# Optimization experiments

Hardware: AMD Instinct MI355X
Metric: run time of the kernel (lower is better)

Reference implementation:

```python
import jax, jax.numpy as jnp
import numpy as np

N = 2048          # num_nodes
A = 100           # anchor count (hard-coded in _select_anchor_points)


def setup_inputs() -> dict:
    key = jax.random.key(0)
    k1, k2, k3 = jax.random.split(key, 3)
    motifGraph = jax.random.uniform(k1, (N, N), dtype=jnp.float32)
    node_weights = jax.random.uniform(k2, (N,), dtype=jnp.float32)
    weight_matrix = jax.random.uniform(k3, (N, A), dtype=jnp.float32)
    sigma = jnp.array(1.0, dtype=jnp.float32)
    return {"motifGraph": motifGraph, "node_weights": node_weights,
            "weight_matrix": weight_matrix, "sigma": sigma}


def _floyd_warshall(w):
    # w: [n,n] edge-weight matrix (inf = no edge, 0 on diagonal)
    n = w.shape[0]
    def step(d, k):
        # d_ij = min(d_ij, d_ik + d_kj)
        d = jnp.minimum(d, d[:, k][:, None] + d[k, :][None, :])
        return d, None
    d, _ = jax.lax.scan(step, w, jnp.arange(n))
    return d


def reference(motifGraph, node_weights, weight_matrix, sigma):
    n = motifGraph.shape[0]
    # _adjust_motif_graph: row-scale by node weights. The original detaches
    # before the scipy floyd_warshall call, so no grad flows through it.
    adj = jax.lax.stop_gradient(motifGraph * node_weights[:n, None])
    # csr_matrix semantics: zero entries are "no edge"; directed=False takes
    # the min of w_ij and w_ji; diagonal distance is 0.
    w = jnp.where(adj > 0, adj, jnp.inf)
    w = jnp.minimum(w, w.T)
    idx = jnp.arange(n)
    w = w.at[idx, idx].set(0.0)
    dist = _floyd_warshall(w)
    dist = jnp.where(jnp.isinf(dist), 100.0, dist)
    # _select_anchor_points: top-100 node weights (all indices < n here)
    anchors = jnp.argsort(-jax.lax.stop_gradient(node_weights))[:A]
    consensus_vectors = dist[:, anchors]                      # [n, A]
    distance_sums = (consensus_vectors.sum(axis=1) - 100.0).sum() / (n * A)
    weighted = weight_matrix[:n, :] * consensus_vectors       # [n, A]
    # build_consensus_graph: cdist(...)**4 == (squared euclidean dist)**2
    xx = jnp.sum(weighted * weighted, axis=1)                 # [n]
    sq = jnp.maximum(xx[:, None] + xx[None, :] - 2.0 * weighted @ weighted.T, 0.0)
    consensus_graph = jnp.exp(-(sq * sq) / (2.0 * sigma ** 2))
    return consensus_vectors, distance_sums, consensus_graph
```

## Files before the change

### kernel.cpp

```cpp
#include <hip/hip_runtime.h>
#include <stdint.h>

#define NN 2048
#define AA 100
#define NT 32

#define F_DIAG   256
#define F_ROW    512
#define F_COL    1536
#define F_PREROW 2560
#define F_PRECOL 2624

typedef float floatx4 __attribute__((ext_vector_type(4)));

template<bool AL> __device__ __forceinline__ float4 ld4(const float* __restrict__ p) {
  if (AL) return *(const float4*)p;
  return make_float4(p[0], p[1], p[2], p[3]);
}
template<bool AL> __device__ __forceinline__ void st4(float* __restrict__ p, float4 v) {
  if (AL) { *(float4*)p = v; }
  else { p[0] = v.x; p[1] = v.y; p[2] = v.z; p[3] = v.w; }
}

__device__ __forceinline__ void minplus16(const float (*A)[68], const float (*B)[68],
                                          float c[4][4], int i0, int j0) {
#pragma unroll 4
  for (int k4 = 0; k4 < 16; ++k4) {
    const int k = k4 * 4;
    float4 a0 = *(const float4*)&A[i0 + 0][k];
    float4 a1 = *(const float4*)&A[i0 + 1][k];
    float4 a2 = *(const float4*)&A[i0 + 2][k];
    float4 a3 = *(const float4*)&A[i0 + 3][k];
    float4 b0 = *(const float4*)&B[k + 0][j0];
    float4 b1 = *(const float4*)&B[k + 1][j0];
    float4 b2 = *(const float4*)&B[k + 2][j0];
    float4 b3 = *(const float4*)&B[k + 3][j0];
#define MP1(ii, jj, f)                                                           \
    c[ii][jj] = fminf(fminf(fminf(fminf(c[ii][jj], a##ii.x + b0.f),              \
                                  a##ii.y + b1.f),                               \
                            a##ii.z + b2.f),                                     \
                      a##ii.w + b3.f)
#define MP_ROW(ii) MP1(ii, 0, x); MP1(ii, 1, y); MP1(ii, 2, z); MP1(ii, 3, w)
    MP_ROW(0); MP_ROW(1); MP_ROW(2); MP_ROW(3);
#undef MP_ROW
#undef MP1
  }
}

__device__ __forceinline__ void close_seq(float (*S)[68], float c[4][4],
                                          int i0, int j0, int ty, int tx) {
  for (int kb = 0; kb < 16; ++kb) {
#pragma unroll
    for (int h = 0; h < 2; ++h) {
      const int k = kb * 4 + h * 2;
      float4 br  = *(const float4*)&S[k][j0];
      float4 br2 = *(const float4*)&S[k + 1][j0];
      float dkk1 = S[k][k + 1];
      float dk1k = S[k + 1][k];
      float a0 = S[i0 + 0][k],     a1 = S[i0 + 1][k],
            a2 = S[i0 + 2][k],     a3 = S[i0 + 3][k];
      float e0 = S[i0 + 0][k + 1], e1 = S[i0 + 1][k + 1],
            e2 = S[i0 + 2][k + 1], e3 = S[i0 + 3][k + 1];
      float4 brp;
      brp.x = fminf(br2.x, dk1k + br.x);
      brp.y = fminf(br2.y, dk1k + br.y);
      brp.z = fminf(br2.z, dk1k + br.z);
      brp.w = fminf(br2.w, dk1k + br.w);
      e0 = fminf(e0, a0 + dkk1);
      e1 = fminf(e1, a1 + dkk1);
      e2 = fminf(e2, a2 + dkk1);
      e3 = fminf(e3, a3 + dkk1);
#define CS2(ii, aa, ee)                                                     \
      c[ii][0] = fminf(fminf(c[ii][0], aa + br.x), ee + brp.x);             \
      c[ii][1] = fminf(fminf(c[ii][1], aa + br.y), ee + brp.y);             \
      c[ii][2] = fminf(fminf(c[ii][2], aa + br.z), ee + brp.z);             \
      c[ii][3] = fminf(fminf(c[ii][3], aa + br.w), ee + brp.w)
      CS2(0, a0, e0); CS2(1, a1, e1); CS2(2, a2, e2); CS2(3, a3, e3);
#undef CS2
      const int kn = k + 2;
      if (kn < 64) {
        const int ow = kn >> 2;
        const int ri = (h == 0) ? 2 : 0;
        if (ow == ty) {
          *(float4*)&S[kn][j0] =
              make_float4(c[ri][0], c[ri][1], c[ri][2], c[ri][3]);
          *(float4*)&S[kn + 1][j0] =
              make_float4(c[ri + 1][0], c[ri + 1][1], c[ri + 1][2], c[ri + 1][3]);
        }
        if (ow == tx) {
          S[i0 + 0][kn] = c[0][ri]; S[i0 + 0][kn + 1] = c[0][ri + 1];
          S[i0 + 1][kn] = c[1][ri]; S[i0 + 1][kn + 1] = c[1][ri + 1];
          S[i0 + 2][kn] = c[2][ri]; S[i0 + 2][kn + 1] = c[2][ri + 1];
          S[i0 + 3][kn] = c[3][ri]; S[i0 + 3][kn + 1] = c[3][ri + 1];
        }
      }
      __syncthreads();
    }
  }
}

template<int LAZY>
__device__ __forceinline__ void waitflag(int* f) {
  if (LAZY == 0) {
    while (__hip_atomic_load(f, __ATOMIC_RELAXED, __HIP_MEMORY_SCOPE_AGENT) == 0) {}
  } else {
    while (__hip_atomic_load(f, __ATOMIC_RELAXED, __HIP_MEMORY_SCOPE_AGENT) == 0)
      __builtin_amdgcn_s_sleep(LAZY);
  }
}
__device__ __forceinline__ void setflag(int* f) {
  __hip_atomic_store(f, 1, __ATOMIC_RELAXED, __HIP_MEMORY_SCOPE_AGENT);
}

__device__ __forceinline__ void stage64(const float* __restrict__ g,
                                        float (*S)[68], int t) {
#pragma unroll
  for (int l = 0; l < 4; ++l) {
    int idx = l * 256 + t;
    int row = idx >> 4, c4 = (idx & 15) * 4;
    *(float4*)&S[row][c4] = *(const float4*)&g[row * 64 + c4];
  }
}
__device__ __forceinline__ void pub64_wt(float* __restrict__ g,
                                         const float c[4][4], int i0, int j0) {
#pragma unroll
  for (int ii = 0; ii < 4; ++ii) {
    floatx4 v = {c[ii][0], c[ii][1], c[ii][2], c[ii][3]};
    float* p = &g[(ii + i0) * 64 + j0];
    asm volatile("global_store_dwordx4 %0, %1, off sc0 sc1"
                 :: "v"(p), "v"(v) : "memory");
  }
  asm volatile("s_waitcnt vmcnt(0)" ::: "memory");
}

__global__ __launch_bounds__(256, 4) void fw_persist(
    const float* __restrict__ mg, const float* __restrict__ nw,
    float* __restrict__ dist, int* __restrict__ Wi,
    float* __restrict__ diagb, float* __restrict__ rowb,
    float* __restrict__ colb, float* __restrict__ prerow,
    float* __restrict__ precol) {
  __shared__ __align__(16) float As[64][68];
  __shared__ __align__(16) float Bs[64][68];
  const int bx = blockIdx.x, by = blockIdx.y;
  const int t = threadIdx.x;
  const int tx = t & 15, ty = t >> 4;
  const int i0 = ty * 4, j0 = tx * 4;
  int* DIAGF   = Wi + F_DIAG;
  int* ROWF    = Wi + F_ROW;
  int* COLF    = Wi + F_COL;
  int* PREROWF = Wi + F_PREROW;
  int* PRECOLF = Wi + F_PRECOL;

#pragma unroll
  for (int l = 0; l < 4; ++l) {
    int idx = l * 256 + t;
    int r = idx >> 4, c4 = (idx & 15) * 4;
    float4 g = *(const float4*)&mg[(bx * 64 + r) * NN + by * 64 + c4];
    Bs[c4 + 0][r] = g.x; Bs[c4 + 1][r] = g.y;
    Bs[c4 + 2][r] = g.z; Bs[c4 + 3][r] = g.w;
  }
  __syncthreads();
  float c[4][4];
  {
    float4 nwj = *(const float4*)&nw[bx * 64 + j0];
#pragma unroll
    for (int ii = 0; ii < 4; ++ii) {
      int rl = i0 + ii;
      int i = by * 64 + rl;
      float nwi = nw[i];
      float4 m = *(const float4*)&mg[i * NN + bx * 64 + j0];
      float4 bt = *(const float4*)&Bs[rl][j0];
      float av[4] = {m.x * nwi, m.y * nwi, m.z * nwi, m.w * nwi};
      float bv[4] = {bt.x * nwj.x, bt.y * nwj.y, bt.z * nwj.z, bt.w * nwj.w};
#pragma unroll
      for (int q = 0; q < 4; ++q) {
        float wa = av[q] > 0.0f ? av[q] : __builtin_huge_valf();
        float wb = bv[q] > 0.0f ? bv[q] : __builtin_huge_valf();
        float v = fminf(wa, wb);
        if (i == bx * 64 + j0 + q) v = 0.0f;
        c[ii][q] = v;
      }
    }
  }
  if ((by == 0 && bx == 1) || (by == 1 && bx == 0)) {
    pub64_wt((by == 0) ? prerow : precol, c, i0, j0);
    __syncthreads();
    if (t == 0) setflag((by == 0) ? PREROWF + 0 : PRECOLF + 0);
  }
  if (bx == 0 && by == 0) {
    __syncthreads();
#pragma unroll
    for (int ii = 0; ii < 4; ++ii)
      *(float4*)&As[i0 + ii][j0] = make_float4(c[ii][0], c[ii][1], c[ii][2], c[ii][3]);
    __syncthreads();
    close_seq(As, c, i0, j0, ty, tx);
    pub64_wt(diagb, c, i0, j0);
    __syncthreads();
    if (t == 0) setflag(DIAGF + 0);
  }

  for (int r = 0; r < NT; ++r) {
    const bool crit = (by == r) || (bx == r) || (by == r + 1) || (bx == r + 1);
    if (crit) __builtin_amdgcn_s_setprio(1);
    else      __builtin_amdgcn_s_setprio(0);
    if (by == r && bx == r) continue;
    const bool closer = (bx == r + 1) && (by == r + 1) && (r + 1 < NT);
    if (closer) {
      if (t == 0) {
        while (__hip_atomic_load(DIAGF + r, __ATOMIC_RELAXED,
                                 __HIP_MEMORY_SCOPE_AGENT) == 0 ||
               __hip_atomic_load(PREROWF + r, __ATOMIC_RELAXED,
                                 __HIP_MEMORY_SCOPE_AGENT) == 0 ||
               __hip_atomic_load(PRECOLF + r, __ATOMIC_RELAXED,
                                 __HIP_MEMORY_SCOPE_AGENT) == 0) {}
      }
      __syncthreads();
      stage64(diagb + r * 4096, As, t);
      stage64(prerow + r * 4096, Bs, t);
      __syncthreads();
      float rp[4][4];
#pragma unroll
      for (int ii = 0; ii < 4; ++ii) {
        float4 q = *(const float4*)&Bs[i0 + ii][j0];
        rp[ii][0] = q.x; rp[ii][1] = q.y; rp[ii][2] = q.z; rp[ii][3] = q.w;
      }
      minplus16(As, Bs, rp, i0, j0);
      __syncthreads();
      stage64(precol + r * 4096, As, t);
#pragma unroll
      for (int ii = 0; ii < 4; ++ii)
        *(float4*)&Bs[i0 + ii][j0] = make_float4(rp[ii][0], rp[ii][1], rp[ii][2], rp[ii][3]);
      __syncthreads();
      minplus16(As, Bs, c, i0, j0);
      __syncthreads();
#pragma unroll
      for (int ii = 0; ii < 4; ++ii)
        *(float4*)&As[i0 + ii][j0] = make_float4(c[ii][0], c[ii][1], c[ii][2], c[ii][3]);
      __syncthreads();
      close_seq(As, c, i0, j0, ty, tx);
      pub64_wt(diagb + (r + 1) * 4096, c, i0, j0);
      __syncthreads();
      if (t == 0) setflag(DIAGF + r + 1);
    } else if (by == r || bx == r) {
      const bool isRow = (by == r);
      __syncthreads();
      float (*Ow)[68] = isRow ? Bs : As;
#pragma unroll
      for (int ii = 0; ii < 4; ++ii)
        *(float4*)&Ow[i0 + ii][j0] =
            make_float4(c[ii][0], c[ii][1], c[ii][2], c[ii][3]);
      if (t == 0) waitflag<0>(DIAGF + r);
      __syncthreads();
      stage64(diagb + r * 4096, isRow ? As : Bs, t);
      __syncthreads();
      minplus16(As, Bs, c, i0, j0);
      float* ob = isRow ? rowb + (r * NT + bx) * 4096
                        : colb + (by * NT + r) * 4096;
      pub64_wt(ob, c, i0, j0);
      __syncthreads();
      if (t == 0) setflag(isRow ? ROWF + r * NT + bx : COLF + by * NT + r);
    } else {
      const bool corner = (r + 2 < NT) &&
          ((by == r + 1 && bx == r + 2) || (by == r + 2 && bx == r + 1));
      const bool near = (by <= r + 2) || (bx <= r + 2);
      if (t == 0) {
        if (corner) {
          waitflag<0>(ROWF + r * NT + bx);
          waitflag<0>(COLF + by * NT + r);
        } else if (near) {
          waitflag<8>(ROWF + r * NT + bx);
          waitflag<8>(COLF + by * NT + r);
        } else {
          waitflag<64>(ROWF + r * NT + bx);
          waitflag<64>(COLF + by * NT + r);
        }
      }
      __syncthreads();
      stage64(colb + (by * NT + r) * 4096, As, t);
      stage64(rowb + (r * NT + bx) * 4096, Bs, t);
      __syncthreads();
      minplus16(As, Bs, c, i0, j0);
      if (corner) {
        const bool isRowC = (by == r + 1);
        pub64_wt((isRowC ? prerow : precol) + (r + 1) * 4096, c, i0, j0);
        __syncthreads();
        if (t == 0) setflag((isRowC ? PREROWF : PRECOLF) + r + 1);
      }
    }
  }
  __builtin_amdgcn_s_setprio(0);

  float* ob = &dist[(by * 64) * NN + bx * 64];
#pragma unroll
  for (int ii = 0; ii < 4; ++ii)
    *(float4*)&ob[(i0 + ii) * NN + j0] =
        make_float4(c[ii][0], c[ii][1], c[ii][2], c[ii][3]);
}

template<bool AL>
__global__ __launch_bounds__(256) void build_w_kernel(
    const float* __restrict__ mg, const float* __restrict__ nw,
    float* __restrict__ w) {
  __shared__ float Tt[64][65];
  __shared__ __align__(16) float As[64][68];
  int bi = blockIdx.y, bj = blockIdx.x;
  int t = threadIdx.x;
  const bool diag0 = (bi == 0) && (bj == 0);
#pragma unroll
  for (int l = 0; l < 4; ++l) {
    int idx = l * 256 + t;
    int r = idx >> 4, c4 = (idx & 15) * 4;
    float4 g = *(const float4*)&mg[(bj * 64 + r) * NN + bi * 64 + c4];
    Tt[c4 + 0][r] = g.x; Tt[c4 + 1][r] = g.y;
    Tt[c4 + 2][r] = g.z; Tt[c4 + 3][r] = g.w;
  }
  __syncthreads();
#pragma unroll
  for (int l = 0; l < 4; ++l) {
    int idx = l * 256 + t;
    int r = idx >> 4, c4 = (idx & 15) * 4;
    int i = bi * 64 + r, j = bj * 64 + c4;
    float4 m = *(const float4*)&mg[i * NN + j];
    float4 nwj = *(const float4*)&nw[j];
    float nwi = nw[i];
    float av[4] = {m.x * nwi, m.y * nwi, m.z * nwi, m.w * nwi};
    float bv[4] = {Tt[r][c4 + 0] * nwj.x, Tt[r][c4 + 1] * nwj.y,
                   Tt[r][c4 + 2] * nwj.z, Tt[r][c4 + 3] * nwj.w};
    float vv[4];
#pragma unroll
    for (int q = 0; q < 4; ++q) {
      float wa = av[q] > 0.0f ? av[q] : __builtin_huge_valf();
      float wb = bv[q] > 0.0f ? bv[q] : __builtin_huge_valf();
      float v = fminf(wa, wb);
      if (i == j + q) v = 0.0f;
      vv[q] = v;
    }
    float4 v4 = make_float4(vv[0], vv[1], vv[2], vv[3]);
    if (diag0) {
      *(float4*)&As[r][c4] = v4;
    } else {
      st4<AL>(&w[i * NN + j], v4);
    }
  }
  if (diag0) {
    __syncthreads();
    int tx = t & 15, ty = t >> 4;
    int i0 = ty * 4, j0 = tx * 4;
    float c[4][4];
#pragma unroll
    for (int ii = 0; ii < 4; ++ii) {
      float4 q = *(const float4*)&As[i0 + ii][j0];
      c[ii][0] = q.x; c[ii][1] = q.y; c[ii][2] = q.z; c[ii][3] = q.w;
    }
    close_seq(As, c, i0, j0, ty, tx);
#pragma unroll
    for (int ii = 0; ii < 4; ++ii)
      st4<AL>(&w[(i0 + ii) * NN + j0],
              make_float4(c[ii][0], c[ii][1], c[ii][2], c[ii][3]));
  }
}

template<bool AL>
__global__ __launch_bounds__(256) void fw_p2(float* __restrict__ d, int r) {
  __shared__ __align__(16) float As[64][68];
  __shared__ __align__(16) float Bs[64][68];
  int tile = blockIdx.x, side = blockIdx.y;
  if (tile == r) return;
  int t = threadIdx.x;
  int dbase = (r * 64) * NN + r * 64;
  int obase = (side == 0) ? (r * 64) * NN + tile * 64
                          : (tile * 64) * NN + r * 64;
  float (*Da)[68] = (side == 0) ? As : Bs;
  float (*Ow)[68] = (side == 0) ? Bs : As;
#pragma unroll
  for (int l = 0; l < 4; ++l) {
    int idx = l * 256 + t;
    int row = idx >> 4, c4 = (idx & 15) * 4;
    *(float4*)&Da[row][c4] = ld4<AL>(&d[dbase + row * NN + c4]);
    *(float4*)&Ow[row][c4] = ld4<AL>(&d[obase + row * NN + c4]);
  }
  int tx = t & 15, ty = t >> 4;
  int i0 = ty * 4, j0 = tx * 4;
  __syncthreads();
  float c[4][4];
#pragma unroll
  for (int ii = 0; ii < 4; ++ii) {
    float4 q = *(const float4*)&Ow[i0 + ii][j0];
    c[ii][0] = q.x; c[ii][1] = q.y; c[ii][2] = q.z; c[ii][3] = q.w;
  }
  minplus16(As, Bs, c, i0, j0);
#pragma unroll
  for (int ii = 0; ii < 4; ++ii)
    st4<AL>(&d[obase + (i0 + ii) * NN + j0],
            make_float4(c[ii][0], c[ii][1], c[ii][2], c[ii][3]));
}

template<bool AL>
__global__ __launch_bounds__(256) void fw_p3(float* __restrict__ d, int r) {
  __shared__ __align__(16) float As[64][68];
  __shared__ __align__(16) float Bs[64][68];
  int bx = blockIdx.x, by = blockIdx.y;
  if (bx == r || by == r) return;
  int t = threadIdx.x;
#pragma unroll
  for (int l = 0; l < 4; ++l) {
    int idx = l * 256 + t;
    int row = idx >> 4, c4 = (idx & 15) * 4;
    *(float4*)&As[row][c4] = ld4<AL>(&d[(by * 64 + row) * NN + r * 64 + c4]);
    *(float4*)&Bs[row][c4] = ld4<AL>(&d[(r * 64 + row) * NN + bx * 64 + c4]);
  }
  int tx = t & 15, ty = t >> 4;
  int i0 = ty * 4, j0 = tx * 4;
  int obase = (by * 64) * NN + bx * 64;
  float c[4][4];
#pragma unroll
  for (int ii = 0; ii < 4; ++ii) {
    float4 q = ld4<AL>(&d[obase + (i0 + ii) * NN + j0]);
    c[ii][0] = q.x; c[ii][1] = q.y; c[ii][2] = q.z; c[ii][3] = q.w;
  }
  __syncthreads();
  minplus16(As, Bs, c, i0, j0);

  bool closer = (bx == r + 1) && (by == r + 1) && (r + 1 < NT);
  if (closer) {
    __syncthreads();
#pragma unroll
    for (int ii = 0; ii < 4; ++ii)
      *(float4*)&As[i0 + ii][j0] = make_float4(c[ii][0], c[ii][1], c[ii][2], c[ii][3]);
    __syncthreads();
    close_seq(As, c, i0, j0, ty, tx);
  }
#pragma unroll
  for (int ii = 0; ii < 4; ++ii)
    st4<AL>(&d[obase + (i0 + ii) * NN + j0],
            make_float4(c[ii][0], c[ii][1], c[ii][2], c[ii][3]));
}

__global__ __launch_bounds__(256) void anchors_kernel(
    const float* __restrict__ nw, int* __restrict__ anchors) {
  __shared__ __align__(16) float s[NN];
  int t = threadIdx.x;
#pragma unroll
  for (int l = 0; l < NN / 256; ++l) s[l * 256 + t] = nw[l * 256 + t];
  __syncthreads();
  int i = blockIdx.x * 64 + (t >> 2);
  int q = t & 3;
  float wi = s[i];
  int rank = 0;
  int jb = q * (NN / 4);
  for (int j = jb; j < jb + NN / 4; j += 4) {
    float4 v = *(const float4*)&s[j];
    rank += (int)(v.x > wi) + ((int)(v.x == wi) & (int)(j + 0 < i));
    rank += (int)(v.y > wi) + ((int)(v.y == wi) & (int)(j + 1 < i));
    rank += (int)(v.z > wi) + ((int)(v.z == wi) & (int)(j + 2 < i));
    rank += (int)(v.w > wi) + ((int)(v.w == wi) & (int)(j + 3 < i));
  }
  rank += __shfl_xor(rank, 1);
  rank += __shfl_xor(rank, 2);
  if (q == 0 && rank < AA) anchors[rank] = i;
}

__global__ __launch_bounds__(256) void cv_kernel(
    const float* __restrict__ dist, const int* __restrict__ anchors,
    float* __restrict__ cv_out, float* __restrict__ sum_acc) {
  int idx = blockIdx.x * 256 + threadIdx.x;
  int i = idx / 100, a = idx - i * 100;
  float dv = dist[i * NN + anchors[a]];
  if (isinf(dv)) dv = 100.0f;
  cv_out[idx] = dv;
  float v = dv;
#pragma unroll
  for (int off = 32; off > 0; off >>= 1) v += __shfl_down(v, off);
  __shared__ float sv[4];
  int lane = threadIdx.x & 63, w = threadIdx.x >> 6;
  if (lane == 0) sv[w] = v;
  __syncthreads();
  if (threadIdx.x == 0) atomicAdd(sum_acc, sv[0] + sv[1] + sv[2] + sv[3]);
}

__global__ __launch_bounds__(256) void graph_kernel(
    const float* __restrict__ wm, const float* __restrict__ cv,
    const float* __restrict__ sigma, float* __restrict__ graph) {
  __shared__ __align__(16) float As[64][108];
  __shared__ __align__(16) float Bs[64][108];
  __shared__ float xs[64], ys[64];
  int bx = blockIdx.x, by = blockIdx.y;
  int t = threadIdx.x;
#pragma unroll
  for (int l = 0; l < 7; ++l) {
    int idx = l * 256 + t;
    if (idx < 1600) {
      int row = idx / 25, c4 = (idx - row * 25) * 4;
      float4 wa = *(const float4*)&wm[(by * 64 + row) * AA + c4];
      float4 ca = *(const float4*)&cv[(by * 64 + row) * AA + c4];
      *(float4*)&As[row][c4] =
          make_float4(wa.x * ca.x, wa.y * ca.y, wa.z * ca.z, wa.w * ca.w);
      float4 wb = *(const float4*)&wm[(bx * 64 + row) * AA + c4];
      float4 cb = *(const float4*)&cv[(bx * 64 + row) * AA + c4];
      *(float4*)&Bs[row][c4] =
          make_float4(wb.x * cb.x, wb.y * cb.y, wb.z * cb.z, wb.w * cb.w);
    }
  }
  __syncthreads();
  if (t < 64) {
    float s = 0.0f;
    for (int k4 = 0; k4 < 25; ++k4) {
      float4 q = *(const float4*)&As[t][k4 * 4];
      s += q.x * q.x + q.y * q.y + q.z * q.z + q.w * q.w;
    }
    xs[t] = s;
  } else if (t < 128) {
    int r = t - 64;
    float s = 0.0f;
    for (int k4 = 0; k4 < 25; ++k4) {
      float4 q = *(const float4*)&Bs[r][k4 * 4];
      s += q.x * q.x + q.y * q.y + q.z * q.z + q.w * q.w;
    }
    ys[r] = s;
  }
  __syncthreads();
  int tx = t & 15, ty = t >> 4;
  float acc[4][4] = {{0.0f}};
#pragma unroll 5
  for (int k4 = 0; k4 < 25; ++k4) {
    int k = k4 * 4;
    float4 a_[4], b_[4];
#pragma unroll
    for (int ii = 0; ii < 4; ++ii) a_[ii] = *(const float4*)&As[ty + 16 * ii][k];
#pragma unroll
    for (int jj = 0; jj < 4; ++jj) b_[jj] = *(const float4*)&Bs[tx + 16 * jj][k];
#pragma unroll
    for (int ii = 0; ii < 4; ++ii)
#pragma unroll
      for (int jj = 0; jj < 4; ++jj)
        acc[ii][jj] += a_[ii].x * b_[jj].x + a_[ii].y * b_[jj].y +
                       a_[ii].z * b_[jj].z + a_[ii].w * b_[jj].w;
  }
  float s = *sigma;
  float inv2s2 = 0.5f / (s * s);
#pragma unroll
  for (int ii = 0; ii < 4; ++ii) {
    int gi = by * 64 + ty + 16 * ii;
    float xi = xs[ty + 16 * ii];
#pragma unroll
    for (int jj = 0; jj < 4; ++jj) {
      int gj = bx * 64 + tx + 16 * jj;
      float sq = fmaxf(xi + ys[tx + 16 * jj] - 2.0f * acc[ii][jj], 0.0f);
      graph[gi * NN + gj] = __expf(-(sq * sq) * inv2s2);
    }
  }
}

__global__ void finalize_kernel(const float* __restrict__ sum_acc,
                                float* __restrict__ out) {
  if (threadIdx.x == 0)
    *out = (*sum_acc - 204800.0f) / 204800.0f;
}

template<bool AL>
static void run_fw_fallback(const float* mg, const float* nw, float* dist,
                            hipStream_t stream) {
  build_w_kernel<AL><<<dim3(NT, NT), 256, 0, stream>>>(mg, nw, dist);
  for (int r = 0; r < NT; ++r) {
    fw_p2<AL><<<dim3(NT, 2), 256, 0, stream>>>(dist, r);
    fw_p3<AL><<<dim3(NT, NT), 256, 0, stream>>>(dist, r);
  }
}

static bool coop_ok() {
  static int ok = -1;
  if (ok < 0) {
    int dev = 0;
    (void)hipGetDevice(&dev);
    int coopAttr = 0;
    (void)hipDeviceGetAttribute(&coopAttr, hipDeviceAttributeCooperativeLaunch, dev);
    int cus = 0;
    (void)hipDeviceGetAttribute(&cus, hipDeviceAttributeMultiprocessorCount, dev);
    int nb = 0;
    hipError_t e = hipOccupancyMaxActiveBlocksPerMultiprocessor(&nb, fw_persist, 256, 0);
    ok = (e == hipSuccess && coopAttr && nb > 0 && (long)nb * cus >= NT * NT) ? 1 : 0;
  }
  return ok == 1;
}

extern "C" void kernel_launch(void* const* d_in, const int* in_sizes, int n_in,
                              void* d_out, int out_size, void* d_ws, size_t ws_size,
                              hipStream_t stream) {
  (void)in_sizes; (void)n_in; (void)out_size;
  const float* mg    = (const float*)d_in[0];
  const float* nw    = (const float*)d_in[1];
  const float* wm    = (const float*)d_in[2];
  const float* sigma = (const float*)d_in[3];
  float* out        = (float*)d_out;
  float* cv_out     = out;
  float* scalar_out = out + 204800;
  float* graph_out  = out + 204801;

  float* W = (float*)d_ws;
  float* sum_acc = W;
  int* anchors   = (int*)(W + 4);
  const size_t needP = (size_t)(16384 + (size_t)NN * NN + 3 * NT * 4096 +
                                2 * (size_t)NT * NT * 4096) * sizeof(float);
  const bool bigP  = ws_size >= needP;
  const bool bigF  = ws_size >= (size_t)(2048 + (size_t)NN * NN) * sizeof(float);
  float* dist = bigP ? (W + 16384) : (bigF ? (W + 2048) : graph_out);
  const bool al = ((((uintptr_t)dist) & 15) == 0);

  (void)hipMemsetAsync(W, 0, 16384, stream);

  bool launched = false;
  if (bigP && al && coop_ok()) {
    int* Wi = (int*)W;
    float* diagb  = dist + (size_t)NN * NN;
    float* rowb   = diagb + NT * 4096;
    float* colb   = rowb + (size_t)NT * NT * 4096;
    float* prerow = colb + (size_t)NT * NT * 4096;
    float* precol = prerow + NT * 4096;
    void* args[] = {(void*)&mg, (void*)&nw, (void*)&dist, (void*)&Wi,
                    (void*)&diagb, (void*)&rowb, (void*)&colb,
                    (void*)&prerow, (void*)&precol};
    hipError_t ce = hipLaunchCooperativeKernel(fw_persist, dim3(NT, NT),
                                               dim3(256, 1, 1), args, 0, stream);
    launched = (ce == hipSuccess);
  }
  if (!launched) {
    if (al) run_fw_fallback<true>(mg, nw, dist, stream);
    else    run_fw_fallback<false>(mg, nw, dist, stream);
  }

  anchors_kernel<<<NN / 64, 256, 0, stream>>>(nw, anchors);
  cv_kernel<<<800, 256, 0, stream>>>(dist, anchors, cv_out, sum_acc);
  graph_kernel<<<dim3(NT, NT), 256, 0, stream>>>(wm, cv_out, sigma, graph_out);
  finalize_kernel<<<1, 64, 0, stream>>>(sum_acc, scalar_out);
}
```

Baseline: 922.3 us.

## Block diagonal closure into 4-wide steps and prioritize critical-path tiles

```diff
diff --git a/kernel.cpp b/kernel.cpp
--- a/kernel.cpp
+++ b/kernel.cpp
@@ -50,52 +50,69 @@
 __device__ __forceinline__ void close_seq(float (*S)[68], float c[4][4],
                                           int i0, int j0, int ty, int tx) {
   for (int kb = 0; kb < 16; ++kb) {
-#pragma unroll
-    for (int h = 0; h < 2; ++h) {
-      const int k = kb * 4 + h * 2;
-      float4 br  = *(const float4*)&S[k][j0];
-      float4 br2 = *(const float4*)&S[k + 1][j0];
-      float dkk1 = S[k][k + 1];
-      float dk1k = S[k + 1][k];
-      float a0 = S[i0 + 0][k],     a1 = S[i0 + 1][k],
-            a2 = S[i0 + 2][k],     a3 = S[i0 + 3][k];
-      float e0 = S[i0 + 0][k + 1], e1 = S[i0 + 1][k + 1],
-            e2 = S[i0 + 2][k + 1], e3 = S[i0 + 3][k + 1];
-      float4 brp;
-      brp.x = fminf(br2.x, dk1k + br.x);
-      brp.y = fminf(br2.y, dk1k + br.y);
-      brp.z = fminf(br2.z, dk1k + br.z);
-      brp.w = fminf(br2.w, dk1k + br.w);
-      e0 = fminf(e0, a0 + dkk1);
-      e1 = fminf(e1, a1 + dkk1);
-      e2 = fminf(e2, a2 + dkk1);
-      e3 = fminf(e3, a3 + dkk1);
-#define CS2(ii, aa, ee)                                                     \
-      c[ii][0] = fminf(fminf(c[ii][0], aa + br.x), ee + brp.x);             \
-      c[ii][1] = fminf(fminf(c[ii][1], aa + br.y), ee + brp.y);             \
-      c[ii][2] = fminf(fminf(c[ii][2], aa + br.z), ee + brp.z);             \
-      c[ii][3] = fminf(fminf(c[ii][3], aa + br.w), ee + brp.w)
-      CS2(0, a0, e0); CS2(1, a1, e1); CS2(2, a2, e2); CS2(3, a3, e3);
-#undef CS2
-      const int kn = k + 2;
-      if (kn < 64) {
-        const int ow = kn >> 2;
-        const int ri = (h == 0) ? 2 : 0;
-        if (ow == ty) {
-          *(float4*)&S[kn][j0] =
-              make_float4(c[ri][0], c[ri][1], c[ri][2], c[ri][3]);
-          *(float4*)&S[kn + 1][j0] =
-              make_float4(c[ri + 1][0], c[ri + 1][1], c[ri + 1][2], c[ri + 1][3]);
-        }
-        if (ow == tx) {
-          S[i0 + 0][kn] = c[0][ri]; S[i0 + 0][kn + 1] = c[0][ri + 1];
-          S[i0 + 1][kn] = c[1][ri]; S[i0 + 1][kn + 1] = c[1][ri + 1];
-          S[i0 + 2][kn] = c[2][ri]; S[i0 + 2][kn + 1] = c[2][ri + 1];
-          S[i0 + 3][kn] = c[3][ri]; S[i0 + 3][kn + 1] = c[3][ri + 1];
-        }
-      }
-      __syncthreads();
-    }
+    const int k = kb * 4;
+    float4 a0 = *(const float4*)&S[i0 + 0][k];
+    float4 a1 = *(const float4*)&S[i0 + 1][k];
+    float4 a2 = *(const float4*)&S[i0 + 2][k];
+    float4 a3 = *(const float4*)&S[i0 + 3][k];
+    float4 b0 = *(const float4*)&S[k + 0][j0];
+    float4 b1 = *(const float4*)&S[k + 1][j0];
+    float4 b2 = *(const float4*)&S[k + 2][j0];
+    float4 b3 = *(const float4*)&S[k + 3][j0];
+    float D[4][4];
+#pragma unroll
+    for (int u = 0; u < 4; ++u) {
+      float4 d = *(const float4*)&S[k + u][k];
+      D[u][0] = d.x; D[u][1] = d.y; D[u][2] = d.z; D[u][3] = d.w;
+    }
+#pragma unroll
+    for (int s = 0; s < 4; ++s)
+#pragma unroll
+      for (int u = 0; u < 4; ++u)
+#pragma unroll
+        for (int v = 0; v < 4; ++v)
+          D[u][v] = fminf(D[u][v], D[u][s] + D[s][v]);
+    float4 R[4];
+#pragma unroll
+    for (int v = 0; v < 4; ++v) {
+      R[v].x = fminf(fminf(D[v][0] + b0.x, D[v][1] + b1.x),
+                     fminf(D[v][2] + b2.x, D[v][3] + b3.x));
+      R[v].y = fminf(fminf(D[v][0] + b0.y, D[v][1] + b1.y),
+                     fminf(D[v][2] + b2.y, D[v][3] + b3.y));
+      R[v].z = fminf(fminf(D[v][0] + b0.z, D[v][1] + b1.z),
+                     fminf(D[v][2] + b2.z, D[v][3] + b3.z));
+      R[v].w = fminf(fminf(D[v][0] + b0.w, D[v][1] + b1.w),
+                     fminf(D[v][2] + b2.w, D[v][3] + b3.w));
+    }
+#define CQ(q, aq)                                                           \
+    {                                                                       \
+      float cv0 = fminf(fminf(aq.x + D[0][0], aq.y + D[1][0]),              \
+                        fminf(aq.z + D[2][0], aq.w + D[3][0]));             \
+      float cv1 = fminf(fminf(aq.x + D[0][1], aq.y + D[1][1]),              \
+                        fminf(aq.z + D[2][1], aq.w + D[3][1]));             \
+      float cv2 = fminf(fminf(aq.x + D[0][2], aq.y + D[1][2]),              \
+                        fminf(aq.z + D[2][2], aq.w + D[3][2]));             \
+      float cv3 = fminf(fminf(aq.x + D[0][3], aq.y + D[1][3]),              \
+                        fminf(aq.z + D[2][3], aq.w + D[3][3]));             \
+      c[q][0] = fminf(c[q][0], fminf(fminf(cv0 + R[0].x, cv1 + R[1].x),     \
+                                     fminf(cv2 + R[2].x, cv3 + R[3].x)));   \
+      c[q][1] = fminf(c[q][1], fminf(fminf(cv0 + R[0].y, cv1 + R[1].y),     \
+                                     fminf(cv2 + R[2].y, cv3 + R[3].y)));   \
+      c[q][2] = fminf(c[q][2], fminf(fminf(cv0 + R[0].z, cv1 + R[1].z),     \
+                                     fminf(cv2 + R[2].z, cv3 + R[3].z)));   \
+      c[q][3] = fminf(c[q][3], fminf(fminf(cv0 + R[0].w, cv1 + R[1].w),     \
+                                     fminf(cv2 + R[2].w, cv3 + R[3].w)));   \
+    }
+    CQ(0, a0) CQ(1, a1) CQ(2, a2) CQ(3, a3)
+#undef CQ
+    const int ow = kb + 1;
+    if (kb < 15 && (ty == ow || tx == ow)) {
+#pragma unroll
+      for (int q = 0; q < 4; ++q)
+        *(float4*)&S[i0 + q][j0] =
+            make_float4(c[q][0], c[q][1], c[q][2], c[q][3]);
+    }
+    __syncthreads();
   }
 }
 
@@ -206,17 +223,13 @@
     if (by == r && bx == r) continue;
     const bool closer = (bx == r + 1) && (by == r + 1) && (r + 1 < NT);
     if (closer) {
-      if (t == 0) {
-        while (__hip_atomic_load(DIAGF + r, __ATOMIC_RELAXED,
-                                 __HIP_MEMORY_SCOPE_AGENT) == 0 ||
-               __hip_atomic_load(PREROWF + r, __ATOMIC_RELAXED,
-                                 __HIP_MEMORY_SCOPE_AGENT) == 0 ||
-               __hip_atomic_load(PRECOLF + r, __ATOMIC_RELAXED,
-                                 __HIP_MEMORY_SCOPE_AGENT) == 0) {}
-      }
+      __builtin_amdgcn_s_setprio(3);
+      if (t == 0) { waitflag<0>(PREROWF + r); waitflag<0>(PRECOLF + r); }
+      __syncthreads();
+      stage64(prerow + r * 4096, Bs, t);
+      if (t == 0) waitflag<0>(DIAGF + r);
       __syncthreads();
       stage64(diagb + r * 4096, As, t);
-      stage64(prerow + r * 4096, Bs, t);
       __syncthreads();
       float rp[4][4];
 #pragma unroll
@@ -262,9 +275,11 @@
     } else {
       const bool corner = (r + 2 < NT) &&
           ((by == r + 1 && bx == r + 2) || (by == r + 2 && bx == r + 1));
-      const bool near = (by <= r + 2) || (bx <= r + 2);
+      const bool nextcloser = (by == r + 2) && (bx == r + 2);
+      const bool near = (by > r && by <= r + 2) || (bx > r && bx <= r + 2);
+      if (corner || nextcloser) __builtin_amdgcn_s_setprio(2);
       if (t == 0) {
-        if (corner) {
+        if (corner || nextcloser) {
           waitflag<0>(ROWF + r * NT + bx);
           waitflag<0>(COLF + by * NT + r);
         } else if (near) {
```

Result: slower. 1.147 ms (+24.4%).

## Dedicate block (0,0) to closing all diagonal tiles on the critical path

Applied to the files above, without the earlier changes.

```diff
diff --git a/kernel.cpp b/kernel.cpp
--- a/kernel.cpp
+++ b/kernel.cpp
@@ -5,11 +5,12 @@
 #define AA 100
 #define NT 32
 
-#define F_DIAG   256
-#define F_ROW    512
-#define F_COL    1536
-#define F_PREROW 2560
-#define F_PRECOL 2624
+#define F_DIAG    256
+#define F_ROW     512
+#define F_COL     1536
+#define F_PREROW  2560
+#define F_PRECOL  2624
+#define F_PREDIAG 2688
 
 typedef float floatx4 __attribute__((ext_vector_type(4)));
 
@@ -97,6 +98,10 @@
       __syncthreads();
     }
   }
+#pragma unroll
+  for (int ii = 0; ii < 4; ++ii)
+    *(float4*)&S[i0 + ii][j0] = make_float4(c[ii][0], c[ii][1], c[ii][2], c[ii][3]);
+  __syncthreads();
 }
 
 template<int LAZY>
@@ -138,18 +143,19 @@
     float* __restrict__ dist, int* __restrict__ Wi,
     float* __restrict__ diagb, float* __restrict__ rowb,
     float* __restrict__ colb, float* __restrict__ prerow,
-    float* __restrict__ precol) {
+    float* __restrict__ precol, float* __restrict__ prediag) {
   __shared__ __align__(16) float As[64][68];
   __shared__ __align__(16) float Bs[64][68];
   const int bx = blockIdx.x, by = blockIdx.y;
   const int t = threadIdx.x;
   const int tx = t & 15, ty = t >> 4;
   const int i0 = ty * 4, j0 = tx * 4;
-  int* DIAGF   = Wi + F_DIAG;
-  int* ROWF    = Wi + F_ROW;
-  int* COLF    = Wi + F_COL;
-  int* PREROWF = Wi + F_PREROW;
-  int* PRECOLF = Wi + F_PRECOL;
+  int* DIAGF    = Wi + F_DIAG;
+  int* ROWF     = Wi + F_ROW;
+  int* COLF     = Wi + F_COL;
+  int* PREROWF  = Wi + F_PREROW;
+  int* PRECOLF  = Wi + F_PRECOL;
+  int* PREDIAGF = Wi + F_PREDIAG;
 
 #pragma unroll
   for (int l = 0; l < 4; ++l) {
@@ -187,6 +193,12 @@
     __syncthreads();
     if (t == 0) setflag((by == 0) ? PREROWF + 0 : PRECOLF + 0);
   }
+  if (by == 1 && bx == 1) {
+    pub64_wt(prediag, c, i0, j0);
+    __syncthreads();
+    if (t == 0) setflag(PREDIAGF + 0);
+  }
+
   if (bx == 0 && by == 0) {
     __syncthreads();
 #pragma unroll
@@ -197,51 +209,88 @@
     pub64_wt(diagb, c, i0, j0);
     __syncthreads();
     if (t == 0) setflag(DIAGF + 0);
+    __builtin_amdgcn_s_setprio(2);
+
+    for (int r = 0; r < NT - 1; ++r) {
+      if (t == 0) {
+        waitflag<0>(PREROWF + r);
+        waitflag<0>(PRECOLF + r);
+        waitflag<0>(PREDIAGF + r);
+      }
+      __syncthreads();
+      float cd[4][4];
+      {
+        const float* pd = prediag + r * 4096;
+#pragma unroll
+        for (int ii = 0; ii < 4; ++ii) {
+          float4 q = *(const float4*)&pd[(i0 + ii) * 64 + j0];
+          cd[ii][0] = q.x; cd[ii][1] = q.y; cd[ii][2] = q.z; cd[ii][3] = q.w;
+        }
+      }
+      stage64(prerow + r * 4096, Bs, t);
+      __syncthreads();
+      float rp[4][4];
+#pragma unroll
+      for (int ii = 0; ii < 4; ++ii) {
+        float4 q = *(const float4*)&Bs[i0 + ii][j0];
+        rp[ii][0] = q.x; rp[ii][1] = q.y; rp[ii][2] = q.z; rp[ii][3] = q.w;
+      }
+      minplus16(As, Bs, rp, i0, j0);
+      __syncthreads();
+#pragma unroll
+      for (int ii = 0; ii < 4; ++ii)
+        *(float4*)&As[i0 + ii][j0] = make_float4(rp[ii][0], rp[ii][1], rp[ii][2], rp[ii][3]);
+      stage64(precol + r * 4096, Bs, t);
+      __syncthreads();
+      minplus16(Bs, As, cd, i0, j0);
+      __syncthreads();
+#pragma unroll
+      for (int ii = 0; ii < 4; ++ii)
+        *(float4*)&As[i0 + ii][j0] = make_float4(cd[ii][0], cd[ii][1], cd[ii][2], cd[ii][3]);
+      __syncthreads();
+      close_seq(As, cd, i0, j0, ty, tx);
+      pub64_wt(diagb + (r + 1) * 4096, cd, i0, j0);
+      __syncthreads();
+      if (t == 0) setflag(DIAGF + r + 1);
+    }
+    __builtin_amdgcn_s_setprio(0);
+
+    for (int r = 1; r < NT; ++r) {
+      if (t == 0) {
+        waitflag<8>(COLF + 0 * NT + r);
+        waitflag<8>(ROWF + r * NT + 0);
+      }
+      __syncthreads();
+      stage64(colb + (0 * NT + r) * 4096, As, t);
+      stage64(rowb + (r * NT + 0) * 4096, Bs, t);
+      __syncthreads();
+      minplus16(As, Bs, c, i0, j0);
+      __syncthreads();
+    }
+    float* ob = &dist[0];
+#pragma unroll
+    for (int ii = 0; ii < 4; ++ii)
+      *(float4*)&ob[(i0 + ii) * NN + j0] =
+          make_float4(c[ii][0], c[ii][1], c[ii][2], c[ii][3]);
+    return;
   }
 
   for (int r = 0; r < NT; ++r) {
     const bool crit = (by == r) || (bx == r) || (by == r + 1) || (bx == r + 1);
     if (crit) __builtin_amdgcn_s_setprio(1);
     else      __builtin_amdgcn_s_setprio(0);
-    if (by == r && bx == r) continue;
-    const bool closer = (bx == r + 1) && (by == r + 1) && (r + 1 < NT);
-    if (closer) {
-      if (t == 0) {
-        while (__hip_atomic_load(DIAGF + r, __ATOMIC_RELAXED,
-                                 __HIP_MEMORY_SCOPE_AGENT) == 0 ||
-               __hip_atomic_load(PREROWF + r, __ATOMIC_RELAXED,
-                                 __HIP_MEMORY_SCOPE_AGENT) == 0 ||
-               __hip_atomic_load(PRECOLF + r, __ATOMIC_RELAXED,
-                                 __HIP_MEMORY_SCOPE_AGENT) == 0) {}
-      }
-      __syncthreads();
-      stage64(diagb + r * 4096, As, t);
-      stage64(prerow + r * 4096, Bs, t);
-      __syncthreads();
-      float rp[4][4];
+    if (by == r && bx == r) {
+      if (t == 0) waitflag<4>(DIAGF + r);
+      __syncthreads();
+      const float* db = diagb + r * 4096;
 #pragma unroll
       for (int ii = 0; ii < 4; ++ii) {
-        float4 q = *(const float4*)&Bs[i0 + ii][j0];
-        rp[ii][0] = q.x; rp[ii][1] = q.y; rp[ii][2] = q.z; rp[ii][3] = q.w;
-      }
-      minplus16(As, Bs, rp, i0, j0);
-      __syncthreads();
-      stage64(precol + r * 4096, As, t);
-#pragma unroll
-      for (int ii = 0; ii < 4; ++ii)
-        *(float4*)&Bs[i0 + ii][j0] = make_float4(rp[ii][0], rp[ii][1], rp[ii][2], rp[ii][3]);
-      __syncthreads();
-      minplus16(As, Bs, c, i0, j0);
-      __syncthreads();
-#pragma unroll
-      for (int ii = 0; ii < 4; ++ii)
-        *(float4*)&As[i0 + ii][j0] = make_float4(c[ii][0], c[ii][1], c[ii][2], c[ii][3]);
-      __syncthreads();
-      close_seq(As, c, i0, j0, ty, tx);
-      pub64_wt(diagb + (r + 1) * 4096, c, i0, j0);
-      __syncthreads();
-      if (t == 0) setflag(DIAGF + r + 1);
-    } else if (by == r || bx == r) {
+        float4 q = *(const float4*)&db[(i0 + ii) * 64 + j0];
+        c[ii][0] = q.x; c[ii][1] = q.y; c[ii][2] = q.z; c[ii][3] = q.w;
+      }
+      continue;
+    }
+    if (by == r || bx == r) {
       const bool isRow = (by == r);
       __syncthreads();
       float (*Ow)[68] = isRow ? Bs : As;
@@ -262,9 +311,11 @@
     } else {
       const bool corner = (r + 2 < NT) &&
           ((by == r + 1 && bx == r + 2) || (by == r + 2 && bx == r + 1));
-      const bool near = (by <= r + 2) || (bx <= r + 2);
+      const bool prediagpub = (r + 2 < NT) && (by == r + 2) && (bx == r + 2);
+      const bool near = (by > r && by <= r + 2) || (bx > r && bx <= r + 2);
+      if (corner || prediagpub) __builtin_amdgcn_s_setprio(2);
       if (t == 0) {
-        if (corner) {
+        if (corner || prediagpub) {
           waitflag<0>(ROWF + r * NT + bx);
           waitflag<0>(COLF + by * NT + r);
         } else if (near) {
@@ -285,6 +336,11 @@
         pub64_wt((isRowC ? prerow : precol) + (r + 1) * 4096, c, i0, j0);
         __syncthreads();
         if (t == 0) setflag((isRowC ? PREROWF : PRECOLF) + r + 1);
+      }
+      if (prediagpub) {
+        pub64_wt(prediag + (r + 1) * 4096, c, i0, j0);
+        __syncthreads();
+        if (t == 0) setflag(PREDIAGF + r + 1);
       }
     }
   }
@@ -599,7 +655,7 @@
   float* W = (float*)d_ws;
   float* sum_acc = W;
   int* anchors   = (int*)(W + 4);
-  const size_t needP = (size_t)(16384 + (size_t)NN * NN + 3 * NT * 4096 +
+  const size_t needP = (size_t)(16384 + (size_t)NN * NN + 4 * NT * 4096 +
                                 2 * (size_t)NT * NT * 4096) * sizeof(float);
   const bool bigP  = ws_size >= needP;
   const bool bigF  = ws_size >= (size_t)(2048 + (size_t)NN * NN) * sizeof(float);
@@ -611,14 +667,15 @@
   bool launched = false;
   if (bigP && al && coop_ok()) {
     int* Wi = (int*)W;
-    float* diagb  = dist + (size_t)NN * NN;
-    float* rowb   = diagb + NT * 4096;
-    float* colb   = rowb + (size_t)NT * NT * 4096;
-    float* prerow = colb + (size_t)NT * NT * 4096;
-    float* precol = prerow + NT * 4096;
+    float* diagb   = dist + (size_t)NN * NN;
+    float* rowb    = diagb + NT * 4096;
+    float* colb    = rowb + (size_t)NT * NT * 4096;
+    float* prerow  = colb + (size_t)NT * NT * 4096;
+    float* precol  = prerow + NT * 4096;
+    float* prediag = precol + NT * 4096;
     void* args[] = {(void*)&mg, (void*)&nw, (void*)&dist, (void*)&Wi,
                     (void*)&diagb, (void*)&rowb, (void*)&colb,
-                    (void*)&prerow, (void*)&precol};
+                    (void*)&prerow, (void*)&precol, (void*)&prediag};
     hipError_t ce = hipLaunchCooperativeKernel(fw_persist, dim3(NT, NT),
                                                dim3(256, 1, 1), args, 0, stream);
     launched = (ce == hipSuccess);
```

Result: slower. 991.4 us (+7.5%).
